# Kernel optimization log

Hardware: AMD Instinct MI355X
Metric: run time of the kernel (lower is better)

Reference implementation:

```python
import jax, jax.numpy as jnp
import numpy as np

NEG_NUM = -10000.0


def setup_inputs() -> dict:
    key = jax.random.key(0)
    ks = jax.random.split(key, 7)
    B, L, M, H, A = 32, 2048, 512, 512, 256
    memory = jax.random.normal(ks[0], (B, L, M), dtype=jnp.float32)
    hidden = jax.random.normal(ks[1], (B, H), dtype=jnp.float32)
    mask = jax.random.randint(ks[2], (B, L), 0, 2, dtype=jnp.int32)
    # ensure no fully-masked row (softmax well-defined)
    mask = mask.at[:, 0].set(1)
    # nn.Linear params: W1 (A, M+H), b1 (A,), W2 (1, A), b2 (1,)
    lim1 = 1.0 / np.sqrt(M + H)
    W1 = jax.random.uniform(ks[3], (A, M + H), jnp.float32, -lim1, lim1)
    b1 = jax.random.uniform(ks[4], (A,), jnp.float32, -lim1, lim1)
    lim2 = 1.0 / np.sqrt(A)
    W2 = jax.random.uniform(ks[5], (1, A), jnp.float32, -lim2, lim2)
    b2 = jax.random.uniform(ks[6], (1,), jnp.float32, -lim2, lim2)
    return {"memory": memory, "hidden": hidden, "mask": mask,
            "W1": W1, "b1": b1, "W2": W2, "b2": b2}


def reference(memory, hidden, mask, W1, b1, W2, b2):
    # memory: (B, L, M), hidden: (B, H)
    M = memory.shape[-1]
    # Split W1 so we never materialize the concat: equivalent to
    # Linear(cat([memory, hidden_expanded])) since cat@W1^T = mem@W1m^T + hid@W1h^T
    W1m, W1h = W1[:, :M], W1[:, M:]
    proj = (jnp.einsum('blm,am->bla', memory, W1m)
            + jnp.einsum('bh,ah->ba', hidden, W1h)[:, None, :]
            + b1)                                   # (B, L, A)
    score = jnp.einsum('bla,a->bl', jnp.tanh(proj), W2[0]) + b2[0]  # (B, L)
    score = jnp.where(mask == 0, NEG_NUM, score)
    p_memory = jax.nn.softmax(score, axis=-1)        # (B, L)
    expected_memory = jnp.einsum('bl,blm->bm', p_memory, memory)  # (B, M)
    return expected_memory, p_memory
```

## Files before the change

### kernel.cpp

```cpp
#include <hip/hip_runtime.h>
#include <hip/hip_bf16.h>

constexpr int Bb = 32;
constexpr int Ll = 2048;
constexpr int Mm = 512;
constexpr int Hh = 512;
constexpr int Aa = 256;

typedef __attribute__((ext_vector_type(4))) float f32x4;
typedef __attribute__((ext_vector_type(16))) float f32x16;
typedef __attribute__((ext_vector_type(8))) short short8;
typedef __attribute__((ext_vector_type(4))) unsigned short ushort4v;

__device__ __forceinline__ unsigned short f2bf(float f) {
    __hip_bfloat16 h = __float2bfloat16(f);
    return *reinterpret_cast<unsigned short*>(&h);
}

__device__ __forceinline__ ushort4v cvt4(f32x4 v) {
    ushort4v o;
    o[0] = f2bf(v[0]); o[1] = f2bf(v[1]); o[2] = f2bf(v[2]); o[3] = f2bf(v[3]);
    return o;
}

__device__ __forceinline__ void gload_lds16(const void* g, void* l) {
    __builtin_amdgcn_global_load_lds(
        (const __attribute__((address_space(1))) unsigned int*)g,
        (__attribute__((address_space(3))) unsigned int*)l, 16, 0, 0);
}

__global__ void k_prep(const float* __restrict__ W1, const float* __restrict__ hidden,
                       const float* __restrict__ b1,
                       unsigned short* __restrict__ W1mb, float* __restrict__ hb) {
    const int tid = threadIdx.x;
    if (blockIdx.x < 128) {
        int i = blockIdx.x * 256 + tid;
        int a  = i >> 7;
        int mq = (i & 127) << 2;
        f32x4 v = *reinterpret_cast<const f32x4*>(W1 + (size_t)a * (Mm + Hh) + mq);
        int ks = mq >> 5;
        int kb = mq & 31;
        int kswz = kb ^ ((a & 3) << 3);
        *reinterpret_cast<ushort4v*>(W1mb + (size_t)ks * (Aa * 32) + a * 32 + kswz) = cvt4(v);
    } else {
        int b = blockIdx.x - 128;
        __shared__ float sh[Hh];
        sh[tid]       = hidden[b * Hh + tid];
        sh[tid + 256] = hidden[b * Hh + 256 + tid];
        __syncthreads();
        int a = tid;
        const float* wrow = W1 + (size_t)a * (Mm + Hh) + Mm;
        float acc = b1[a];
        #pragma unroll 8
        for (int h = 0; h < Hh; h += 4) {
            f32x4 w = *reinterpret_cast<const f32x4*>(wrow + h);
            acc += w[0] * sh[h] + w[1] * sh[h + 1] + w[2] * sh[h + 2] + w[3] * sh[h + 3];
        }
        hb[b * Aa + a] = acc;
    }
}

__launch_bounds__(256, 4)
__global__ void k_score(const float* __restrict__ mem,
                        const unsigned short* __restrict__ W1mb,
                        const float* __restrict__ hb, const float* __restrict__ W2,
                        float* __restrict__ score) {
    __shared__ unsigned short ldsA[2][64 * 32];
    __shared__ unsigned short ldsB[2][256 * 32];

    const int tid  = threadIdx.x;
    const int wave = tid >> 6;
    const int lane = tid & 63;
    const int l31  = lane & 31;
    const int hi   = lane >> 5;
    const int blockRow = blockIdx.x * 64;
    const int b = blockRow >> 11;

    f32x16 acc[2][2];
    #pragma unroll
    for (int i = 0; i < 2; i++)
        #pragma unroll
        for (int j = 0; j < 2; j++)
            #pragma unroll
            for (int e = 0; e < 16; e++) acc[i][j][e] = 0.f;

    const int c0 = tid, c1 = tid + 256;
    const int ar0 = c0 >> 3, ak0 = (c0 & 7) * 4;
    const int ar1 = c1 >> 3, ak1 = (c1 & 7) * 4;
    const int sa0 = ar0 * 32 + (ak0 ^ ((ar0 & 3) << 3));
    const int sa1 = ar1 * 32 + (ak1 ^ ((ar1 & 3) << 3));
    const float* gA0 = mem + (size_t)(blockRow + ar0) * Mm + ak0;
    const float* gA1 = mem + (size_t)(blockRow + ar1) * Mm + ak1;
    const char* gB = (const char*)W1mb;

    const int swz = (l31 & 3) << 3;
    const int aoff0 = (hi * 8) ^ swz;
    const int aoff1 = (hi * 8 + 16) ^ swz;
    const int arow0 = l31 * 32;
    const int arow1 = (32 + l31) * 32;
    const int brow0 = (wave * 64 + l31) * 32;
    const int brow1 = (wave * 64 + 32 + l31) * 32;

    #pragma unroll
    for (int j = 0; j < 4; ++j)
        gload_lds16(gB + (size_t)(wave * 4 + j) * 1024 + lane * 16,
                    &ldsB[0][(wave * 4 + j) * 512]);
    {
        f32x4 a0 = *reinterpret_cast<const f32x4*>(gA0);
        f32x4 a1 = *reinterpret_cast<const f32x4*>(gA1);
        *reinterpret_cast<ushort4v*>(&ldsA[0][sa0]) = cvt4(a0);
        *reinterpret_cast<ushort4v*>(&ldsA[0][sa1]) = cvt4(a1);
    }
    f32x4 p0 = *reinterpret_cast<const f32x4*>(gA0 + 32);
    f32x4 p1 = *reinterpret_cast<const f32x4*>(gA1 + 32);
    __syncthreads();

    for (int ks = 0; ks < 16; ++ks) {
        const int cur = ks & 1, nxt = cur ^ 1;
        if (ks < 15) {
            #pragma unroll
            for (int j = 0; j < 4; ++j)
                gload_lds16(gB + (size_t)(ks + 1) * 16384 + (wave * 4 + j) * 1024 + lane * 16,
                            &ldsB[nxt][(wave * 4 + j) * 512]);
            *reinterpret_cast<ushort4v*>(&ldsA[nxt][sa0]) = cvt4(p0);
            *reinterpret_cast<ushort4v*>(&ldsA[nxt][sa1]) = cvt4(p1);
        }
        if (ks < 14) {
            p0 = *reinterpret_cast<const f32x4*>(gA0 + (ks + 2) * 32);
            p1 = *reinterpret_cast<const f32x4*>(gA1 + (ks + 2) * 32);
        }
        const unsigned short* A  = ldsA[cur];
        const unsigned short* Bt = ldsB[cur];
        #pragma unroll
        for (int kk = 0; kk < 2; ++kk) {
            const int ao = kk ? aoff1 : aoff0;
            short8 a0 = *reinterpret_cast<const short8*>(&A[arow0 + ao]);
            short8 a1 = *reinterpret_cast<const short8*>(&A[arow1 + ao]);
            short8 b0 = *reinterpret_cast<const short8*>(&Bt[brow0 + ao]);
            short8 b1 = *reinterpret_cast<const short8*>(&Bt[brow1 + ao]);
            acc[0][0] = __builtin_amdgcn_mfma_f32_32x32x16_bf16(a0, b0, acc[0][0], 0, 0, 0);
            acc[0][1] = __builtin_amdgcn_mfma_f32_32x32x16_bf16(a0, b1, acc[0][1], 0, 0, 0);
            acc[1][0] = __builtin_amdgcn_mfma_f32_32x32x16_bf16(a1, b0, acc[1][0], 0, 0, 0);
            acc[1][1] = __builtin_amdgcn_mfma_f32_32x32x16_bf16(a1, b1, acc[1][1], 0, 0, 0);
        }
        __syncthreads();
    }

    float sc[2][16];
    #pragma unroll
    for (int tr = 0; tr < 2; tr++)
        #pragma unroll
        for (int rg = 0; rg < 16; rg++) sc[tr][rg] = 0.f;
    #pragma unroll
    for (int tc = 0; tc < 2; ++tc) {
        int a = wave * 64 + tc * 32 + l31;
        float hba = hb[b * Aa + a];
        float w2a = W2[a];
        #pragma unroll
        for (int tr = 0; tr < 2; tr++)
            #pragma unroll
            for (int rg = 0; rg < 16; rg++) {
                float pr = acc[tr][tc][rg] + hba;
                float e = __expf(2.f * pr);
                float t = (e - 1.f) * __builtin_amdgcn_rcpf(e + 1.f);
                sc[tr][rg] += t * w2a;
            }
    }
    #pragma unroll
    for (int off = 1; off < 32; off <<= 1)
        #pragma unroll
        for (int tr = 0; tr < 2; tr++)
            #pragma unroll
            for (int rg = 0; rg < 16; rg++)
                sc[tr][rg] += __shfl_xor(sc[tr][rg], off, 64);
    float* sred = (float*)&ldsA[0][0];
    if (l31 == 0) {
        #pragma unroll
        for (int tr = 0; tr < 2; tr++)
            #pragma unroll
            for (int rg = 0; rg < 16; rg++) {
                int row = tr * 32 + (rg & 3) + 8 * (rg >> 2) + 4 * hi;
                sred[row * 4 + wave] = sc[tr][rg];
            }
    }
    __syncthreads();
    if (tid < 64)
        score[blockRow + tid] = sred[tid * 4] + sred[tid * 4 + 1]
                              + sred[tid * 4 + 2] + sred[tid * 4 + 3];
}

__launch_bounds__(256)
__global__ void k_exp1(const float* __restrict__ mem, const float* __restrict__ score,
                       const int* __restrict__ mask,
                       float* __restrict__ p, float* __restrict__ partial) {
    const int b   = blockIdx.x >> 5;
    const int lc  = blockIdx.x & 31;
    const int tid = threadIdx.x;
    const int wave = tid >> 6;
    __shared__ float redmx[4];
    __shared__ float redsm[4];
    __shared__ float sp[64];
    __shared__ f32x4 sacc[128];

    const float* sb = score + b * Ll;
    const int*   mb = mask + b * Ll;

    float v[8]; int mk[8];
    #pragma unroll
    for (int i = 0; i < 8; i++) {
        int l = i * 256 + tid;
        v[i]  = sb[l];
        mk[i] = mb[l];
    }
    float mx = -1e30f;
    #pragma unroll
    for (int i = 0; i < 8; i++) if (mk[i]) mx = fmaxf(mx, v[i]);
    #pragma unroll
    for (int off = 1; off < 64; off <<= 1) mx = fmaxf(mx, __shfl_xor(mx, off, 64));
    if ((tid & 63) == 0) redmx[wave] = mx;
    __syncthreads();
    mx = fmaxf(fmaxf(redmx[0], redmx[1]), fmaxf(redmx[2], redmx[3]));

    float s = 0.f;
    #pragma unroll
    for (int i = 0; i < 8; i++) s += mk[i] ? __expf(v[i] - mx) : 0.f;
    #pragma unroll
    for (int off = 1; off < 64; off <<= 1) s += __shfl_xor(s, off, 64);
    if ((tid & 63) == 0) redsm[wave] = s;
    __syncthreads();
    s = redsm[0] + redsm[1] + redsm[2] + redsm[3];
    const float inv = 1.f / s;

    if (tid < 64) {
        int l = lc * 64 + tid;
        float pv = mb[l] ? __expf(sb[l] - mx) * inv : 0.f;
        sp[tid] = pv;
        p[b * Ll + l] = pv;
    }
    __syncthreads();

    const int half = tid >> 7, cq = tid & 127;
    const float* base = mem + ((size_t)b * Ll + lc * 64) * Mm + cq * 4;
    f32x4 acc = (f32x4){0.f, 0.f, 0.f, 0.f};
    #pragma unroll 8
    for (int rr = half; rr < 64; rr += 2)
        acc += sp[rr] * *reinterpret_cast<const f32x4*>(base + (size_t)rr * Mm);
    if (half == 1) sacc[cq] = acc;
    __syncthreads();
    if (half == 0) {
        acc += sacc[cq];
        *reinterpret_cast<f32x4*>(partial + (size_t)blockIdx.x * Mm + cq * 4) = acc;
    }
}

__global__ void k_exp2(const float* __restrict__ partial, float* __restrict__ out) {
    const int b  = blockIdx.x;
    const int mi = threadIdx.x;
    const float* pb = partial + (size_t)b * 32 * Mm + mi * 4;
    f32x4 acc = (f32x4){0.f, 0.f, 0.f, 0.f};
    #pragma unroll 8
    for (int c = 0; c < 32; ++c)
        acc += *reinterpret_cast<const f32x4*>(pb + (size_t)c * Mm);
    *reinterpret_cast<f32x4*>(out + b * Mm + mi * 4) = acc;
}

extern "C" void kernel_launch(void* const* d_in, const int* in_sizes, int n_in,
                              void* d_out, int out_size, void* d_ws, size_t ws_size,
                              hipStream_t stream) {
    const float* memory = (const float*)d_in[0];
    const float* hidden = (const float*)d_in[1];
    const int*   mask   = (const int*)d_in[2];
    const float* W1     = (const float*)d_in[3];
    const float* b1     = (const float*)d_in[4];
    const float* W2     = (const float*)d_in[5];
    float* out = (float*)d_out;

    unsigned short* W1mb = (unsigned short*)d_ws;
    float* hb      = (float*)((char*)d_ws + 256 * 1024);
    float* score   = (float*)((char*)d_ws + 288 * 1024);
    float* partial = (float*)((char*)d_ws + 1024 * 1024);
    float* p = out + Bb * Mm;

    k_prep<<<160, 256, 0, stream>>>(W1, hidden, b1, W1mb, hb);
    k_score<<<1024, 256, 0, stream>>>(memory, W1mb, hb, W2, score);
    k_exp1<<<1024, 256, 0, stream>>>(memory, score, mask, p, partial);
    k_exp2<<<32, 128, 0, stream>>>(partial, out);
}
```

Baseline: 254.1 us.

## Fuse score, local softmax and weighted sum via split-softmax rescaling

```diff
diff --git a/kernel.cpp b/kernel.cpp
--- a/kernel.cpp
+++ b/kernel.cpp
@@ -61,10 +61,12 @@
 }
 
 __launch_bounds__(256, 4)
-__global__ void k_score(const float* __restrict__ mem,
-                        const unsigned short* __restrict__ W1mb,
-                        const float* __restrict__ hb, const float* __restrict__ W2,
-                        float* __restrict__ score) {
+__global__ void k_main(const float* __restrict__ mem,
+                       const unsigned short* __restrict__ W1mb,
+                       const float* __restrict__ hb, const float* __restrict__ W2,
+                       const int* __restrict__ mask,
+                       float* __restrict__ wbuf, float* __restrict__ mxbuf,
+                       float* __restrict__ smbuf, float* __restrict__ partial) {
     __shared__ unsigned short ldsA[2][64 * 32];
     __shared__ unsigned short ldsB[2][256 * 32];
 
@@ -174,6 +176,8 @@
             for (int rg = 0; rg < 16; rg++)
                 sc[tr][rg] += __shfl_xor(sc[tr][rg], off, 64);
     float* sred = (float*)&ldsA[0][0];
+    float* sp   = (float*)&ldsA[1][0];
+    f32x4* sacc = (f32x4*)&ldsB[0][0];
     if (l31 == 0) {
         #pragma unroll
         for (int tr = 0; tr < 2; tr++)
@@ -184,84 +188,68 @@
             }
     }
     __syncthreads();
-    if (tid < 64)
-        score[blockRow + tid] = sred[tid * 4] + sred[tid * 4 + 1]
-                              + sred[tid * 4 + 2] + sred[tid * 4 + 3];
-}
-
-__launch_bounds__(256)
-__global__ void k_exp1(const float* __restrict__ mem, const float* __restrict__ score,
-                       const int* __restrict__ mask,
-                       float* __restrict__ p, float* __restrict__ partial) {
-    const int b   = blockIdx.x >> 5;
-    const int lc  = blockIdx.x & 31;
-    const int tid = threadIdx.x;
-    const int wave = tid >> 6;
-    __shared__ float redmx[4];
-    __shared__ float redsm[4];
-    __shared__ float sp[64];
-    __shared__ f32x4 sacc[128];
-
-    const float* sb = score + b * Ll;
-    const int*   mb = mask + b * Ll;
-
-    float v[8]; int mk[8];
+
+    if (tid < 64) {
+        float sv = sred[tid * 4] + sred[tid * 4 + 1] + sred[tid * 4 + 2] + sred[tid * 4 + 3];
+        int mk = mask[blockRow + tid];
+        float mx = mk ? sv : -1e30f;
+        #pragma unroll
+        for (int off = 1; off < 64; off <<= 1) mx = fmaxf(mx, __shfl_xor(mx, off, 64));
+        float w = mk ? __expf(sv - mx) : 0.f;
+        float sm = w;
+        #pragma unroll
+        for (int off = 1; off < 64; off <<= 1) sm += __shfl_xor(sm, off, 64);
+        sp[tid] = w;
+        wbuf[blockRow + tid] = w;
+        if (tid == 0) { mxbuf[blockIdx.x] = mx; smbuf[blockIdx.x] = sm; }
+    }
+    __syncthreads();
+
+    const int half = tid >> 7, cq = tid & 127;
+    const float* base = mem + (size_t)blockRow * Mm + cq * 4;
+    f32x4 acc4 = (f32x4){0.f, 0.f, 0.f, 0.f};
+    #pragma unroll 8
+    for (int rr = half; rr < 64; rr += 2)
+        acc4 += sp[rr] * *reinterpret_cast<const f32x4*>(base + (size_t)rr * Mm);
+    if (half == 1) sacc[cq] = acc4;
+    __syncthreads();
+    if (half == 0) {
+        acc4 += sacc[cq];
+        *reinterpret_cast<f32x4*>(partial + (size_t)blockIdx.x * Mm + cq * 4) = acc4;
+    }
+}
+
+__global__ void k_final(const float* __restrict__ wbuf, const float* __restrict__ mxbuf,
+                        const float* __restrict__ smbuf, const float* __restrict__ partial,
+                        float* __restrict__ out, float* __restrict__ p) {
+    const int b = blockIdx.x, tid = threadIdx.x;
+    __shared__ float sf[32];
+    if (tid < 32) {
+        float mx = mxbuf[b * 32 + tid];
+        float sm = smbuf[b * 32 + tid];
+        float MX = mx;
+        #pragma unroll
+        for (int off = 1; off < 32; off <<= 1) MX = fmaxf(MX, __shfl_xor(MX, off, 64));
+        float f = __expf(mx - MX);
+        float z = f * sm;
+        #pragma unroll
+        for (int off = 1; off < 32; off <<= 1) z += __shfl_xor(z, off, 64);
+        sf[tid] = f / z;
+    }
+    __syncthreads();
+    const float* wb = wbuf + b * Ll;
     #pragma unroll
     for (int i = 0; i < 8; i++) {
         int l = i * 256 + tid;
-        v[i]  = sb[l];
-        mk[i] = mb[l];
-    }
-    float mx = -1e30f;
-    #pragma unroll
-    for (int i = 0; i < 8; i++) if (mk[i]) mx = fmaxf(mx, v[i]);
-    #pragma unroll
-    for (int off = 1; off < 64; off <<= 1) mx = fmaxf(mx, __shfl_xor(mx, off, 64));
-    if ((tid & 63) == 0) redmx[wave] = mx;
-    __syncthreads();
-    mx = fmaxf(fmaxf(redmx[0], redmx[1]), fmaxf(redmx[2], redmx[3]));
-
-    float s = 0.f;
-    #pragma unroll
-    for (int i = 0; i < 8; i++) s += mk[i] ? __expf(v[i] - mx) : 0.f;
-    #pragma unroll
-    for (int off = 1; off < 64; off <<= 1) s += __shfl_xor(s, off, 64);
-    if ((tid & 63) == 0) redsm[wave] = s;
-    __syncthreads();
-    s = redsm[0] + redsm[1] + redsm[2] + redsm[3];
-    const float inv = 1.f / s;
-
-    if (tid < 64) {
-        int l = lc * 64 + tid;
-        float pv = mb[l] ? __expf(sb[l] - mx) * inv : 0.f;
-        sp[tid] = pv;
-        p[b * Ll + l] = pv;
-    }
-    __syncthreads();
-
-    const int half = tid >> 7, cq = tid & 127;
-    const float* base = mem + ((size_t)b * Ll + lc * 64) * Mm + cq * 4;
-    f32x4 acc = (f32x4){0.f, 0.f, 0.f, 0.f};
-    #pragma unroll 8
-    for (int rr = half; rr < 64; rr += 2)
-        acc += sp[rr] * *reinterpret_cast<const f32x4*>(base + (size_t)rr * Mm);
-    if (half == 1) sacc[cq] = acc;
-    __syncthreads();
-    if (half == 0) {
-        acc += sacc[cq];
-        *reinterpret_cast<f32x4*>(partial + (size_t)blockIdx.x * Mm + cq * 4) = acc;
-    }
-}
-
-__global__ void k_exp2(const float* __restrict__ partial, float* __restrict__ out) {
-    const int b  = blockIdx.x;
-    const int mi = threadIdx.x;
-    const float* pb = partial + (size_t)b * 32 * Mm + mi * 4;
-    f32x4 acc = (f32x4){0.f, 0.f, 0.f, 0.f};
-    #pragma unroll 8
-    for (int c = 0; c < 32; ++c)
-        acc += *reinterpret_cast<const f32x4*>(pb + (size_t)c * Mm);
-    *reinterpret_cast<f32x4*>(out + b * Mm + mi * 4) = acc;
+        p[b * Ll + l] = wb[l] * sf[l >> 6];
+    }
+    if (tid < 128) {
+        f32x4 acc = (f32x4){0.f, 0.f, 0.f, 0.f};
+        #pragma unroll 8
+        for (int c = 0; c < 32; ++c)
+            acc += sf[c] * *reinterpret_cast<const f32x4*>(partial + ((size_t)(b * 32 + c)) * Mm + tid * 4);
+        *reinterpret_cast<f32x4*>(out + b * Mm + tid * 4) = acc;
+    }
 }
 
 extern "C" void kernel_launch(void* const* d_in, const int* in_sizes, int n_in,
@@ -277,12 +265,14 @@
 
     unsigned short* W1mb = (unsigned short*)d_ws;
     float* hb      = (float*)((char*)d_ws + 256 * 1024);
-    float* score   = (float*)((char*)d_ws + 288 * 1024);
+    float* wbuf    = (float*)((char*)d_ws + 512 * 1024);
+    float* mxbuf   = (float*)((char*)d_ws + 768 * 1024);
+    float* smbuf   = (float*)((char*)d_ws + 772 * 1024);
     float* partial = (float*)((char*)d_ws + 1024 * 1024);
     float* p = out + Bb * Mm;
 
     k_prep<<<160, 256, 0, stream>>>(W1, hidden, b1, W1mb, hb);
-    k_score<<<1024, 256, 0, stream>>>(memory, W1mb, hb, W2, score);
-    k_exp1<<<1024, 256, 0, stream>>>(memory, score, mask, p, partial);
-    k_exp2<<<32, 128, 0, stream>>>(partial, out);
-}
+    k_main<<<1024, 256, 0, stream>>>(memory, W1mb, hb, W2, mask,
+                                     wbuf, mxbuf, smbuf, partial);
+    k_final<<<32, 256, 0, stream>>>(wbuf, mxbuf, smbuf, partial, out, p);
+}
```

Result: faster. 241.2 us (-5.1%).
